# Kernel optimization log

Hardware: AMD Instinct MI355X
Metric: run time of the kernel (lower is better)

## Reference

```python
import jax, jax.numpy as jnp
import numpy as np

N = 100000
E = 600000
EL = 200000
HID = 16
HEADS = 4
NUM_NODE_TYPES = 8
NUM_EDGE_TYPES = 22
EDGE_DIM = 16


def setup_inputs() -> dict:
    key = jax.random.key(0)
    ks = jax.random.split(key, 32)
    s = 0.1
    d1, d2 = HID, HID * HEADS  # per-head dims of layer1 / layer2
    inp = {
        'x': jax.random.normal(ks[0], (N, HID), jnp.float32),
        'edge_index': jax.random.randint(ks[1], (2, E), 0, N),
        'node_type': jax.random.randint(ks[2], (N,), 0, NUM_NODE_TYPES),
        'edge_attr': jax.random.normal(ks[3], (E, EDGE_DIM), jnp.float32),
        'edge_type': jax.random.randint(ks[4], (E,), 0, NUM_EDGE_TYPES),
        'edge_label_index': jax.random.randint(ks[5], (2, EL), 0, N),
        # ---- layer 1 params (in=HID, heads=4, out-per-head=HID, concat) ----
        'Wx1': jax.random.normal(ks[6], (HID, HEADS * d1)) * s,
        'We1': jax.random.normal(ks[7], (EDGE_DIM, HEADS * d1)) * s,
        'nt1': jax.random.normal(ks[8], (NUM_NODE_TYPES, HID)) * s,
        'et1': jax.random.normal(ks[9], (NUM_EDGE_TYPES, HEADS * d1)) * s,
        'as1': jax.random.normal(ks[10], (HEADS, d1)) * s,
        'ad1': jax.random.normal(ks[11], (HEADS, d1)) * s,
        'ae1': jax.random.normal(ks[12], (HEADS, d1)) * s,
        'res1': jax.random.normal(ks[13], (HID, HEADS * d1)) * s,
        # ---- layer 2 params (in=4*HID, heads=4, out-per-head=4*HID, mean) ----
        'Wx2': jax.random.normal(ks[14], (HEADS * HID, HEADS * d2)) * s,
        'We2': jax.random.normal(ks[15], (EDGE_DIM, HEADS * d2)) * s,
        'nt2': jax.random.normal(ks[16], (NUM_NODE_TYPES, HEADS * HID)) * s,
        'et2': jax.random.normal(ks[17], (NUM_EDGE_TYPES, HEADS * d2)) * s,
        'as2': jax.random.normal(ks[18], (HEADS, d2)) * s,
        'ad2': jax.random.normal(ks[19], (HEADS, d2)) * s,
        'ae2': jax.random.normal(ks[20], (HEADS, d2)) * s,
        # ---- edge decoder (2*4*HID -> 4*HID -> 1) ----
        'W1': jax.random.normal(ks[21], (2 * HEADS * HID, HEADS * HID)) * s,
        'b1': jnp.zeros((HEADS * HID,), jnp.float32),
        'W2': jax.random.normal(ks[22], (HEADS * HID, 1)) * s,
        'b2': jnp.zeros((1,), jnp.float32),
    }
    return inp


def hgat_layer(x, edge_index, node_type, edge_attr, edge_type,
               Wx, We, nt_emb, et_emb, a_s, a_d, a_e, res_W,
               heads, d, concat, n):
    src, dst = edge_index[0], edge_index[1]
    # type-conditioned node projection -> [N, heads, d]
    h = ((x + nt_emb[node_type]) @ Wx).reshape(n, heads, d)
    # type-conditioned edge features -> [E, heads, d]
    e = (edge_attr @ We + et_emb[edge_type]).reshape(-1, heads, d)
    hs = h[src]  # [E, heads, d] gather
    hd = h[dst]
    sc = (jnp.einsum('ehd,hd->eh', hs, a_s)
          + jnp.einsum('ehd,hd->eh', hd, a_d)
          + jnp.einsum('ehd,hd->eh', e, a_e))
    sc = jax.nn.leaky_relu(sc, 0.2)
    # segment softmax over incoming edges of each destination node
    m = jax.ops.segment_max(sc, dst, num_segments=n)
    p = jnp.exp(sc - m[dst])
    den = jax.ops.segment_sum(p, dst, num_segments=n)
    alpha = p / (den[dst] + 1e-16)
    msg = alpha[:, :, None] * (hs + e)  # [E, heads, d]
    out = jax.ops.segment_sum(msg.reshape(-1, heads * d), dst, num_segments=n)
    out = out.reshape(n, heads, d)
    if concat:
        return out.reshape(n, heads * d) + x @ res_W
    else:
        return out.mean(axis=1) + x  # in-dim == out-dim: identity residual


def reference(x, edge_index, node_type, edge_attr, edge_type, edge_label_index,
              Wx1, We1, nt1, et1, as1, ad1, ae1, res1,
              Wx2, We2, nt2, et2, as2, ad2, ae2,
              W1, b1, W2, b2):
    n = x.shape[0]
    z = hgat_layer(x, edge_index, node_type, edge_attr, edge_type,
                   Wx1, We1, nt1, et1, as1, ad1, ae1, res1,
                   HEADS, HID, True, n)
    z = jax.nn.relu(z)
    z = hgat_layer(z, edge_index, node_type, edge_attr, edge_type,
                   Wx2, We2, nt2, et2, as2, ad2, ae2, None,
                   HEADS, HEADS * HID, False, n)
    # edge decoder: gather endpoint embeddings, 2-layer MLP
    row, col = edge_label_index[0], edge_label_index[1]
    zz = jnp.concatenate([z[row], z[col]], axis=-1)  # [EL, 2*4*HID]
    h = jax.nn.relu(zz @ W1 + b1)
    pred = (h @ W2 + b2).reshape(-1)
    return pred, z
```

## Files before the change

kernel.cpp:

```cpp
#include <hip/hip_runtime.h>
#include <stdint.h>

typedef unsigned short u16;
typedef unsigned int   u32;

#define NN  100000
#define NE  600000
#define NEL 200000

__device__ __forceinline__ float b2f(u16 u){ return __uint_as_float(((u32)u)<<16); }
__device__ __forceinline__ u16 f2b(float f){
  u32 u = __float_as_uint(f);
  u32 r = (u + 0x7FFFu + ((u>>16)&1u)) >> 16;
  return (u16)r;
}
__device__ __forceinline__ void unpack8(uint4 v, float* o){
  o[0]=__uint_as_float(v.x<<16); o[1]=__uint_as_float(v.x&0xffff0000u);
  o[2]=__uint_as_float(v.y<<16); o[3]=__uint_as_float(v.y&0xffff0000u);
  o[4]=__uint_as_float(v.z<<16); o[5]=__uint_as_float(v.z&0xffff0000u);
  o[6]=__uint_as_float(v.w<<16); o[7]=__uint_as_float(v.w&0xffff0000u);
}
__device__ __forceinline__ float ldf(const void* p, size_t i, int m){
  return m ? b2f(((const u16*)p)[i]) : ((const float*)p)[i];
}
__device__ __forceinline__ void ld16(const void* p, size_t off, int m, float* o){
  if (m){
    const uint4* q = (const uint4*)((const u16*)p + off);
    uint4 a=q[0], b=q[1]; unpack8(a,o); unpack8(b,o+8);
  } else {
    const float4* q = (const float4*)((const float*)p + off);
    float4 a=q[0],b=q[1],c=q[2],d=q[3];
    o[0]=a.x;o[1]=a.y;o[2]=a.z;o[3]=a.w; o[4]=b.x;o[5]=b.y;o[6]=b.z;o[7]=b.w;
    o[8]=c.x;o[9]=c.y;o[10]=c.z;o[11]=c.w; o[12]=d.x;o[13]=d.y;o[14]=d.z;o[15]=d.w;
  }
}
__device__ __forceinline__ void stf(void* p, size_t i, int m, float v){
  if (m) ((u16*)p)[i] = f2b(v); else ((float*)p)[i] = v;
}
__device__ __forceinline__ void atomAdd(float* p, float v){ unsafeAtomicAdd(p, v); }

__global__ void k_detect(const void* a0,const void* a3,const void* a6,const void* a7,
                         const void* a8,const void* a9,const void* a10,const void* a11,
                         const void* a12,const void* a13,const void* a14,const void* a15,
                         const void* a16,const void* a17,const void* a18,const void* a19,
                         const void* a20,const void* a21,const void* a23,
                         int* __restrict__ flags){
  const void* ptrs[19] = {a0,a3,a6,a7,a8,a9,a10,a11,a12,a13,a14,a15,a16,a17,a18,a19,a20,a21,a23};
  const int  idxs[19] = {0,3,6,7,8,9,10,11,12,13,14,15,16,17,18,19,20,21,23};
  int b = blockIdx.x;
  const u16* q = (const u16*)ptrs[b];
  u16 u = q[threadIdx.x];
  int e = (u>>7)&0xFF;
  bool good = (u==0) || (e>=110 && e<=141);
  unsigned long long m = __ballot(good);
  if (threadIdx.x==0) flags[idxs[b]] = (__popcll(m) >= 52) ? 1 : 0;
}

__global__ __launch_bounds__(256) void k_zero(float* __restrict__ buf, int n){
  int i = blockIdx.x*256 + threadIdx.x;
  if (i < n) buf[i] = 0.f;
}
__global__ __launch_bounds__(256) void k_stub(u16* __restrict__ out, int n){
  int i = blockIdx.x*256 + threadIdx.x;
  if (i < n) out[i] = 0;
}

__global__ __launch_bounds__(256) void k_pack(const void* __restrict__ Wx2,
                                              const int* __restrict__ flags,
                                              u32* __restrict__ Wxp){
  int m14 = flags[14];
  int i = blockIdx.x*256 + threadIdx.x;
  int k2=i>>8, col=i&255;
  u16 lo = f2b(ldf(Wx2,(size_t)(2*k2)*256+col,m14));
  u16 hi = f2b(ldf(Wx2,(size_t)(2*k2+1)*256+col,m14));
  Wxp[i] = ((u32)hi<<16)|lo;
}

__global__ __launch_bounds__(256) void k_hist(const int* __restrict__ ei, int* __restrict__ cnt){
  int e = blockIdx.x*256 + threadIdx.x;
  if (e < NE) atomicAdd(&cnt[ei[NE+e]], 1);
}
__global__ __launch_bounds__(256) void k_scan1(const int* __restrict__ cnt,
                                               int* __restrict__ row_ptr, int* __restrict__ bsum){
  __shared__ int sb[256];
  int i = blockIdx.x*256 + threadIdx.x, t = threadIdx.x;
  int c = (i < NN) ? cnt[i] : 0;
  sb[t] = c; __syncthreads();
  for (int off=1; off<256; off<<=1){
    int v = (t>=off) ? sb[t-off] : 0; __syncthreads();
    sb[t] += v; __syncthreads();
  }
  if (i < NN) row_ptr[i] = sb[t] - c;
  if (t == 255) bsum[blockIdx.x] = sb[255];
}
__global__ __launch_bounds__(512) void k_scan2(const int* __restrict__ bsum, int* __restrict__ boff){
  __shared__ int sb[512];
  int t = threadIdx.x;
  int nblk = (NN+255)/256;
  int c = (t < nblk) ? bsum[t] : 0;
  sb[t] = c; __syncthreads();
  for (int off=1; off<512; off<<=1){
    int v = (t>=off) ? sb[t-off] : 0; __syncthreads();
    sb[t] += v; __syncthreads();
  }
  boff[t] = sb[t] - c;
}
__global__ __launch_bounds__(256) void k_scan3(int* __restrict__ row_ptr, const int* __restrict__ boff){
  int i = blockIdx.x*256 + threadIdx.x;
  if (i < NN) row_ptr[i] += boff[blockIdx.x];
  if (i == 0) row_ptr[NN] = NE;
}
__global__ __launch_bounds__(256) void k_scatter(const int* __restrict__ ei, const int* __restrict__ etype,
                                                 const int* __restrict__ row_ptr,
                                                 int* __restrict__ cur, int* __restrict__ perm,
                                                 int* __restrict__ rank, int* __restrict__ se){
  int e = blockIdx.x*256 + threadIdx.x;
  if (e < NE){
    int d = ei[NE+e];
    int pos = row_ptr[d] + atomicAdd(&cur[d], 1);
    perm[pos] = e;
    rank[e] = pos;
    se[pos] = ei[e] | (etype[e]<<20);
  }
}

__global__ void k_fold(const void* __restrict__ We1, const void* __restrict__ ae1, const void* __restrict__ et1,
                       const void* __restrict__ We2, const void* __restrict__ ae2, const void* __restrict__ et2,
                       const int* __restrict__ flags,
                       float* We1a, float* et1a, float* We2a, float* et2a){
  int m7=flags[7], m12=flags[12], m9=flags[9], m15=flags[15], m20=flags[20], m17=flags[17];
  int t = threadIdx.x;
  if (t < 64){
    int k=t>>2, h=t&3; float s=0.f;
    for (int d=0; d<16; d++) s += ldf(We1,k*64+h*16+d,m7)*ldf(ae1,h*16+d,m12);
    We1a[t]=s;
  } else if (t < 152){
    int i=t-64; int k=i>>2, h=i&3; float s=0.f;
    for (int d=0; d<16; d++) s += ldf(et1,k*64+h*16+d,m9)*ldf(ae1,h*16+d,m12);
    et1a[i]=s;
  } else if (t < 216){
    int i=t-152; int k=i>>2, h=i&3; float s=0.f;
    for (int d=0; d<64; d++) s += ldf(We2,k*256+h*64+d,m15)*ldf(ae2,h*64+d,m20);
    We2a[i]=s;
  } else if (t < 304){
    int i=t-216; int k=i>>2, h=i&3; float s=0.f;
    for (int d=0; d<64; d++) s += ldf(et2,k*256+h*64+d,m17)*ldf(ae2,h*64+d,m20);
    et2a[i]=s;
  }
}

__global__ __launch_bounds__(256) void k1_node(
    const void* __restrict__ x, const int* __restrict__ ntype,
    const void* __restrict__ Wx1, const void* __restrict__ nt1, const void* __restrict__ res1,
    const void* __restrict__ as1, const void* __restrict__ ad1,
    const int* __restrict__ flags,
    float* __restrict__ h1, float* __restrict__ out1,
    float* __restrict__ ssrc1, float* __restrict__ sdst1){
  __shared__ float sWx[1024], sRes[1024], sA[64], sD[64], sNt[128];
  int m0=flags[0], m6=flags[6], m8=flags[8], m13=flags[13], m10=flags[10], m11=flags[11];
  for (int i=threadIdx.x;i<1024;i+=256){ sWx[i]=ldf(Wx1,i,m6); sRes[i]=ldf(res1,i,m13); }
  if (threadIdx.x<64){ sA[threadIdx.x]=ldf(as1,threadIdx.x,m10); sD[threadIdx.x]=ldf(ad1,threadIdx.x,m11); }
  if (threadIdx.x<128) sNt[threadIdx.x]=ldf(nt1,threadIdx.x,m8);
  __syncthreads();
  int n = blockIdx.x*256 + threadIdx.x;
  if (n >= NN) return;
  float xv[16]; ld16(x, (size_t)n*16, m0, xv);
  int nt = ntype[n];
  float xin[16];
  #pragma unroll
  for (int k=0;k<16;k++) xin[k] = xv[k] + sNt[nt*16+k];
  float ss[4]={0,0,0,0}, sd[4]={0,0,0,0};
  #pragma unroll
  for (int jq=0;jq<16;jq++){
    float sarr[4], rarr[4];
    #pragma unroll
    for (int m=0;m<4;m++){
      int j = jq*4+m;
      float s=0.f, r=0.f;
      #pragma unroll
      for (int k=0;k<16;k++){ s += xin[k]*sWx[k*64+j]; r += xv[k]*sRes[k*64+j]; }
      sarr[m]=s; rarr[m]=r;
      ss[j>>4] += s*sA[j];
      sd[j>>4] += s*sD[j];
    }
    ((float4*)(h1  + (size_t)n*64))[jq] = make_float4(sarr[0],sarr[1],sarr[2],sarr[3]);
    ((float4*)(out1+ (size_t)n*64))[jq] = make_float4(rarr[0],rarr[1],rarr[2],rarr[3]);
  }
  ((float4*)ssrc1)[n] = make_float4(ss[0],ss[1],ss[2],ss[3]);
  ((float4*)sdst1)[n] = make_float4(sd[0],sd[1],sd[2],sd[3]);
}

__global__ __launch_bounds__(256) void k_sed(
    const int* __restrict__ ei, const void* __restrict__ eattr, const int* __restrict__ etype,
    const float* __restrict__ Wea, const float* __restrict__ eta,
    const float* __restrict__ ssrc, const float* __restrict__ sdst,
    const int* __restrict__ rank,
    const int* __restrict__ flags,
    float* __restrict__ psort){
  __shared__ float sW[64], sE[88];
  int m3=flags[3];
  if (threadIdx.x<64) sW[threadIdx.x]=Wea[threadIdx.x];
  if (threadIdx.x<88) sE[threadIdx.x]=eta[threadIdx.x];
  __syncthreads();
  int e = blockIdx.x*256 + threadIdx.x;
  if (e >= NE) return;
  int s = ei[e], d = ei[NE+e], t = etype[e];
  float ea[16]; ld16(eattr, (size_t)e*16, m3, ea);
  float4 s4 = ((const float4*)ssrc)[s];
  float4 d4 = ((const float4*)sdst)[d];
  float sv[4] = { s4.x+d4.x, s4.y+d4.y, s4.z+d4.z, s4.w+d4.w };
  float pv[4];
  #pragma unroll
  for (int h=0; h<4; h++){
    float v = sE[t*4+h] + sv[h];
    #pragma unroll
    for (int k=0;k<16;k++) v += ea[k]*sW[k*4+h];
    v = v > 0.f ? v : 0.2f*v;
    v = fminf(v, 60.f);
    pv[h] = __expf(v);
  }
  ((float4*)psort)[rank[e]] = make_float4(pv[0],pv[1],pv[2],pv[3]);
}

__global__ __launch_bounds__(256) void k_msg1(
    const void* __restrict__ eattr, const void* __restrict__ et1,
    const float* __restrict__ h1, const float* __restrict__ psort,
    const int* __restrict__ row_ptr, const int* __restrict__ perm, const int* __restrict__ se,
    const int* __restrict__ flags,
    float* __restrict__ out1, float* __restrict__ gsum1){
  __shared__ float sEt[22*64];
  int m3=flags[3], m9=flags[9];
  for (int i=threadIdx.x;i<22*64;i+=256) sEt[i]=ldf(et1,i,m9);
  __syncthreads();
  int j = threadIdx.x & 63;
  int h = j>>4, jk = j&15;
  int wid = threadIdx.x>>6;
  for (int it=0; it<8; ++it){
    int n = (blockIdx.x*4 + wid)*8 + it;
    int beg=row_ptr[n], end=row_ptr[n+1];
    float sp=0.f, acc=0.f, gacc=0.f;
    int i=beg;
    for (; i+1<end; i+=2){
      int st0=se[i], st1=se[i+1];
      float4 p0=((const float4*)psort)[i], p1=((const float4*)psort)[i+1];
      int pe0=perm[i], pe1=perm[i+1];
      int s0=st0&0xFFFFF, t0=st0>>20;
      int s1=st1&0xFFFFF, t1=st1>>20;
      float ph0 = (h==0?p0.x:h==1?p0.y:h==2?p0.z:p0.w);
      float ph1 = (h==0?p1.x:h==1?p1.y:h==2?p1.z:p1.w);
      float hv0 = h1[(size_t)s0*64+j];
      float hv1 = h1[(size_t)s1*64+j];
      float ea0 = ldf(eattr,(size_t)pe0*16+jk,m3);
      float ea1 = ldf(eattr,(size_t)pe1*16+jk,m3);
      sp   += ph0 + ph1;
      acc  += ph0*(hv0+sEt[t0*64+j]) + ph1*(hv1+sEt[t1*64+j]);
      gacc += ph0*ea0 + ph1*ea1;
    }
    if (i<end){
      int st0=se[i];
      float4 p0=((const float4*)psort)[i];
      int pe0=perm[i];
      int s0=st0&0xFFFFF, t0=st0>>20;
      float ph0 = (h==0?p0.x:h==1?p0.y:h==2?p0.z:p0.w);
      sp   += ph0;
      acc  += ph0*(h1[(size_t)s0*64+j]+sEt[t0*64+j]);
      gacc += ph0*ldf(eattr,(size_t)pe0*16+jk,m3);
    }
    float rd = 1.f/(sp+1e-16f);
    out1[(size_t)n*64+j] += acc*rd;
    gsum1[(size_t)n*64+j] = gacc*rd;
  }
}

__global__ __launch_bounds__(256) void k_fin1(
    const float* __restrict__ gsum1, const void* __restrict__ We1,
    const int* __restrict__ flags, float* __restrict__ out1){
  __shared__ float sW[16*64];
  __shared__ float sG[4][64];
  int m7=flags[7];
  for (int i=threadIdx.x;i<16*64;i+=256) sW[i]=ldf(We1,i,m7);
  __syncthreads();
  int slot=threadIdx.x>>6, j=threadIdx.x&63;
  int h = j>>4;
  for (int nb=blockIdx.x; nb<NN/4; nb+=gridDim.x){
    int n = nb*4 + slot;
    sG[slot][j] = gsum1[(size_t)n*64 + j];
    float s=0.f;
    #pragma unroll
    for (int k=0;k<16;k++) s += sG[slot][h*16+k]*sW[k*64+j];
    out1[(size_t)n*64+j] += s;
  }
}

__global__ __launch_bounds__(256) void k5_node2(
    const int* __restrict__ ntype,
    const u32* __restrict__ Wxp, const void* __restrict__ nt2,
    const void* __restrict__ as2, const void* __restrict__ ad2,
    const int* __restrict__ flags,
    const float* __restrict__ out1, float* __restrict__ zfin,
    u16* __restrict__ h2, float* __restrict__ ssrc2, float* __restrict__ sdst2){
  __shared__ u32   sWp[32*256];
  __shared__ float sNt[512];
  __shared__ float sAs[256], sAd[256];
  __shared__ float sZ[4][8][64];
  __shared__ float sR[4][2][256];
  int m16=flags[16], m18=flags[18], m19=flags[19];
  for (int i=threadIdx.x;i<32*256;i+=256) sWp[i] = Wxp[i];
  for (int i=threadIdx.x;i<512;i+=256) sNt[i]=ldf(nt2,i,m16);
  sAs[threadIdx.x]=ldf(as2,threadIdx.x,m18);
  sAd[threadIdx.x]=ldf(ad2,threadIdx.x,m19);
  __syncthreads();
  int slot=threadIdx.x>>6, j=threadIdx.x&63;
  int base=(blockIdx.x*4+slot)*8;
  #pragma unroll
  for (int i=0;i<8;i++){
    int n=base+i;
    float z = out1[(size_t)n*64+j]; z = fmaxf(z, 0.f);
    zfin[(size_t)n*64+j] = z;
    sZ[slot][i][j] = z + sNt[(ntype[n]<<6)|j];
  }
  __syncthreads();
  float acc[8][4];
  #pragma unroll
  for (int i=0;i<8;i++){ acc[i][0]=0;acc[i][1]=0;acc[i][2]=0;acc[i][3]=0; }
  for (int k2=0;k2<32;k2++){
    u32 w0p=sWp[k2*256+j], w1p=sWp[k2*256+64+j], w2p=sWp[k2*256+128+j], w3p=sWp[k2*256+192+j];
    float w0l=__uint_as_float(w0p<<16), w0h=__uint_as_float(w0p&0xffff0000u);
    float w1l=__uint_as_float(w1p<<16), w1h=__uint_as_float(w1p&0xffff0000u);
    float w2l=__uint_as_float(w2p<<16), w2h=__uint_as_float(w2p&0xffff0000u);
    float w3l=__uint_as_float(w3p<<16), w3h=__uint_as_float(w3p&0xffff0000u);
    #pragma unroll
    for (int i=0;i<8;i++){
      float2 zz = *(const float2*)&sZ[slot][i][k2*2];
      acc[i][0] += zz.x*w0l + zz.y*w0h;
      acc[i][1] += zz.x*w1l + zz.y*w1h;
      acc[i][2] += zz.x*w2l + zz.y*w2h;
      acc[i][3] += zz.x*w3l + zz.y*w3h;
    }
  }
  int g=j>>4, l=j&15;
  #pragma unroll
  for (int i=0;i<8;i++){
    int n=base+i;
    u32 lo = (u32)f2b(acc[i][0]) | ((u32)f2b(acc[i][1])<<16);
    u32 hi = (u32)f2b(acc[i][2]) | ((u32)f2b(acc[i][3])<<16);
    *(uint2*)&h2[(size_t)n*256 + j*4] = make_uint2(lo,hi);
    sR[slot][0][      j] = acc[i][0]*sAs[      j];
    sR[slot][0][ 64 + j] = acc[i][1]*sAs[ 64 + j];
    sR[slot][0][128 + j] = acc[i][2]*sAs[128 + j];
    sR[slot][0][192 + j] = acc[i][3]*sAs[192 + j];
    sR[slot][1][      j] = acc[i][0]*sAd[      j];
    sR[slot][1][ 64 + j] = acc[i][1]*sAd[ 64 + j];
    sR[slot][1][128 + j] = acc[i][2]*sAd[128 + j];
    sR[slot][1][192 + j] = acc[i][3]*sAd[192 + j];
    float4 v4 = *(const float4*)&sR[slot][0][g*64 + l*4];
    float4 w4 = *(const float4*)&sR[slot][1][g*64 + l*4];
    float vs = v4.x+v4.y+v4.z+v4.w;
    float vd = w4.x+w4.y+w4.z+w4.w;
    #pragma unroll
    for (int off=1; off<16; off<<=1){ vs += __shfl_xor(vs,off); vd += __shfl_xor(vd,off); }
    if (l==0){ ssrc2[(size_t)n*4+g]=vs; sdst2[(size_t)n*4+g]=vd; }
  }
}

__global__ __launch_bounds__(256) void k_msg2(
    const void* __restrict__ eattr, const void* __restrict__ et2,
    const u16* __restrict__ h2, const float* __restrict__ psort,
    const int* __restrict__ row_ptr, const int* __restrict__ perm, const int* __restrict__ se,
    const int* __restrict__ flags,
    float* __restrict__ zfin, float* __restrict__ gsum){
  __shared__ float4 sEt4[22*64];
  int m3=flags[3], m17=flags[17];
  for (int i=threadIdx.x;i<22*64;i+=256){
    int t=i>>6, j=i&63;
    sEt4[i] = make_float4(ldf(et2,(size_t)t*256+j,m17),      ldf(et2,(size_t)t*256+64+j,m17),
                          ldf(et2,(size_t)t*256+128+j,m17),  ldf(et2,(size_t)t*256+192+j,m17));
  }
  __syncthreads();
  int j = threadIdx.x & 63;
  int jh = j>>4, jk = j&15;
  int wid = threadIdx.x>>6;
  for (int it=0; it<8; ++it){
    int n = (blockIdx.x*4 + wid)*8 + it;
    int beg=row_ptr[n], end=row_ptr[n+1];
    float ds0=0,ds1=0,ds2=0,ds3=0;
    float pa0=0,pa1=0,pa2=0,pa3=0, gacc=0;
    int i=beg;
    for (; i+1<end; i+=2){
      int st0=se[i], st1=se[i+1];
      float4 q0=((const float4*)psort)[i], q1=((const float4*)psort)[i+1];
      int pe0=perm[i], pe1=perm[i+1];
      int s0=st0&0xFFFFF, t0=st0>>20;
      int s1=st1&0xFFFFF, t1=st1>>20;
      uint2 hA = *(const uint2*)&h2[(size_t)s0*256 + j*4];
      uint2 hB = *(const uint2*)&h2[(size_t)s1*256 + j*4];
      float ea0 = ldf(eattr,(size_t)pe0*16+jk,m3);
      float ea1 = ldf(eattr,(size_t)pe1*16+jk,m3);
      float4 eA = sEt4[t0*64+j], eB = sEt4[t1*64+j];
      ds0 += q0.x+q1.x; ds1 += q0.y+q1.y; ds2 += q0.z+q1.z; ds3 += q0.w+q1.w;
      pa0 += q0.x*(__uint_as_float(hA.x<<16)        +eA.x) + q1.x*(__uint_as_float(hB.x<<16)        +eB.x);
      pa1 += q0.y*(__uint_as_float(hA.x&0xffff0000u)+eA.y) + q1.y*(__uint_as_float(hB.x&0xffff0000u)+eB.y);
      pa2 += q0.z*(__uint_as_float(hA.y<<16)        +eA.z) + q1.z*(__uint_as_float(hB.y<<16)        +eB.z);
      pa3 += q0.w*(__uint_as_float(hA.y&0xffff0000u)+eA.w) + q1.w*(__uint_as_float(hB.y&0xffff0000u)+eB.w);
      float pj0 = (jh==0?q0.x:jh==1?q0.y:jh==2?q0.z:q0.w);
      float pj1 = (jh==0?q1.x:jh==1?q1.y:jh==2?q1.z:q1.w);
      gacc += pj0*ea0 + pj1*ea1;
    }
    if (i<end){
      int st0=se[i];
      float4 q0=((const float4*)psort)[i];
      int pe0=perm[i];
      int s0=st0&0xFFFFF, t0=st0>>20;
      uint2 hA = *(const uint2*)&h2[(size_t)s0*256 + j*4];
      float4 eA = sEt4[t0*64+j];
      ds0 += q0.x; ds1 += q0.y; ds2 += q0.z; ds3 += q0.w;
      pa0 += q0.x*(__uint_as_float(hA.x<<16)        +eA.x);
      pa1 += q0.y*(__uint_as_float(hA.x&0xffff0000u)+eA.y);
      pa2 += q0.z*(__uint_as_float(hA.y<<16)        +eA.z);
      pa3 += q0.w*(__uint_as_float(hA.y&0xffff0000u)+eA.w);
      float pj0 = (jh==0?q0.x:jh==1?q0.y:jh==2?q0.z:q0.w);
      gacc += pj0*ldf(eattr,(size_t)pe0*16+jk,m3);
    }
    float r0=1.f/(ds0+1e-16f), r1=1.f/(ds1+1e-16f), r2=1.f/(ds2+1e-16f), r3=1.f/(ds3+1e-16f);
    float acc = pa0*r0 + pa1*r1 + pa2*r2 + pa3*r3;
    float rj = (jh==0?r0:jh==1?r1:jh==2?r2:r3);
    zfin[(size_t)n*64+j] += 0.25f*acc;
    gsum[(size_t)n*64+j] = gacc*rj;
  }
}

__global__ __launch_bounds__(256) void k_fin(
    const float* __restrict__ gsum, const void* __restrict__ We2,
    const int* __restrict__ flags, float* __restrict__ zfin){
  __shared__ float sW[16*256];
  __shared__ float sG[4][64];
  int m15=flags[15];
  for (int i=threadIdx.x;i<16*256;i+=256) sW[i]=ldf(We2,i,m15);
  __syncthreads();
  int slot=threadIdx.x>>6, j=threadIdx.x&63;
  for (int nb=blockIdx.x; nb<NN/4; nb+=gridDim.x){
    int n = nb*4 + slot;
    sG[slot][j] = gsum[(size_t)n*64 + j];
    float acc = 0.f;
    #pragma unroll
    for (int h=0;h<4;h++){
      float s=0.f;
      #pragma unroll
      for (int k=0;k<16;k++) s += sG[slot][h*16+k]*sW[k*256 + h*64 + j];
      acc += s;
    }
    zfin[(size_t)n*64+j] += 0.25f*acc;
  }
}

__global__ __launch_bounds__(256) void k_zout(const float* __restrict__ zf, void* __restrict__ out,
                                              const int* __restrict__ flags){
  int mo = flags[0];
  int i = blockIdx.x*256 + threadIdx.x;
  if (i < NN*64) stf(out, (size_t)NEL + i, mo, zf[i]);
}

__global__ __launch_bounds__(256) void k_dec(
    const int* __restrict__ eli, const float* __restrict__ zfin,
    const void* __restrict__ W1, const u16* __restrict__ b1,
    const void* __restrict__ W2, const u16* __restrict__ b2,
    const int* __restrict__ flags,
    void* __restrict__ out){
  __shared__ float sW1[128*64];
  __shared__ float sB1[64], sW2[64];
  __shared__ float sZZ[4][8][128];
  int m21=flags[21], m23=flags[23], mo=flags[0];
  for (int i=threadIdx.x;i<128*64;i+=256) sW1[i]=ldf(W1,i,m21);
  if (threadIdx.x<64){ sB1[threadIdx.x]=b2f(b1[threadIdx.x]); sW2[threadIdx.x]=ldf(W2,threadIdx.x,m23); }
  __syncthreads();
  float b2v = b2f(b2[0]);
  int slot=threadIdx.x>>6, j=threadIdx.x&63;
  int ngrp=(NEL+7)/8;
  for (int g0 = blockIdx.x*4; g0 < ngrp; g0 += gridDim.x*4){
    int g = g0 + slot;
    bool active = (g < ngrp);
    int e0 = active ? g*8 : 0;
    int cnt = active ? ((NEL - e0) < 8 ? (NEL - e0) : 8) : 0;
    #pragma unroll
    for (int q=0;q<8;q++){
      int qq = (q<cnt) ? q : 0;
      int r=eli[e0+qq], c=eli[NEL+e0+qq];
      sZZ[slot][q][j]    = zfin[(size_t)r*64+j];
      sZZ[slot][q][64+j] = zfin[(size_t)c*64+j];
    }
    __syncthreads();
    float acc[8];
    #pragma unroll
    for (int q=0;q<8;q++) acc[q]=sB1[j];
    for (int k4=0;k4<32;k4++){
      float w0=sW1[(k4*4+0)*64+j], w1=sW1[(k4*4+1)*64+j];
      float w2=sW1[(k4*4+2)*64+j], w3=sW1[(k4*4+3)*64+j];
      #pragma unroll
      for (int q=0;q<8;q++){
        float4 zz = *(const float4*)&sZZ[slot][q][k4*4];
        acc[q] += zz.x*w0 + zz.y*w1 + zz.z*w2 + zz.w*w3;
      }
    }
    #pragma unroll
    for (int q=0;q<8;q++){
      float a = fmaxf(acc[q],0.f)*sW2[j];
      #pragma unroll
      for (int off=32; off; off>>=1) a += __shfl_xor(a,off);
      if (j==0 && q<cnt) stf(out, e0+q, mo, a + b2v);
    }
    __syncthreads();
  }
}

extern "C" void kernel_launch(void* const* d_in, const int* in_sizes, int n_in,
                              void* d_out, int out_size, void* d_ws, size_t ws_size,
                              hipStream_t stream){
  (void)in_sizes; (void)n_in;
  const void* x    =d_in[0];
  const int* ei    =(const int*)d_in[1];
  const int* ntype =(const int*)d_in[2];
  const void* eattr=d_in[3];
  const int* etype =(const int*)d_in[4];
  const int* eli   =(const int*)d_in[5];
  const void* Wx1=d_in[6];  const void* We1=d_in[7];  const void* nt1=d_in[8];
  const void* et1=d_in[9];  const void* as1=d_in[10]; const void* ad1=d_in[11];
  const void* ae1=d_in[12]; const void* res1=d_in[13];
  const void* Wx2=d_in[14]; const void* We2=d_in[15]; const void* nt2=d_in[16];
  const void* et2=d_in[17]; const void* as2=d_in[18]; const void* ad2=d_in[19];
  const void* ae2=d_in[20];
  const void* W1=d_in[21];  const u16* b1=(const u16*)d_in[22];
  const void* W2=d_in[23];  const u16* b2=(const u16*)d_in[24];

  const size_t NEED_BYTES = 30809572ULL * 4ULL;
  if (ws_size < NEED_BYTES){
    k_stub<<<(out_size+255)/256,256,0,stream>>>((u16*)d_out, out_size);
    return;
  }
  float* ws=(float*)d_ws;
  size_t o=0;
  int*   flags=(int*)(ws+o); o+=32;
  float* We1a =ws+o; o+=64;
  float* et1a =ws+o; o+=96;
  float* We2a =ws+o; o+=64;
  float* et2a =ws+o; o+=96;
  int*   cnt    =(int*)(ws+o); o+=NN;
  int*   row_ptr=(int*)(ws+o); o+=NN+4;
  int*   perm   =(int*)(ws+o); o+=NE;
  int*   bsum   =(int*)(ws+o); o+=512;
  int*   boff   =(int*)(ws+o); o+=512;
  int*   rank   =(int*)(ws+o); o+=NE;
  int*   se     =(int*)(ws+o); o+=NE;
  u32*   Wxp    =(u32*)(ws+o); o+=8192;
  float* ssrc =ws+o; o+=(size_t)NN*4;
  float* sdst =ws+o; o+=(size_t)NN*4;
  float* psort=ws+o; o+=(size_t)NE*4;
  float* slotA=ws+o; o+=(size_t)NN*64;
  float* out1 =ws+o; o+=(size_t)NN*64;
  u16*   h2   =(u16*)(ws+o); o+=(size_t)NN*128;
  float* h1   = slotA;
  float* zfin = slotA;
  float* gsum = out1;
  float* gsum1= (float*)h2;

  const int NBLK = (NN+255)/256;

  k_detect<<<19,64,0,stream>>>(x,eattr,Wx1,We1,nt1,et1,as1,ad1,ae1,res1,
                               Wx2,We2,nt2,et2,as2,ad2,ae2,W1,W2,flags);
  k_fold<<<1,320,0,stream>>>(We1,ae1,et1,We2,ae2,et2,flags,We1a,et1a,We2a,et2a);
  k_pack<<<32,256,0,stream>>>(Wx2,flags,Wxp);
  k_zero<<<(NN+255)/256,256,0,stream>>>((float*)cnt, NN);
  k_hist<<<(NE+255)/256,256,0,stream>>>(ei, cnt);
  k_scan1<<<NBLK,256,0,stream>>>(cnt, row_ptr, bsum);
  k_scan2<<<1,512,0,stream>>>(bsum, boff);
  k_scan3<<<NBLK,256,0,stream>>>(row_ptr, boff);
  k_zero<<<(NN+255)/256,256,0,stream>>>((float*)cnt, NN);
  k_scatter<<<(NE+255)/256,256,0,stream>>>(ei, etype, row_ptr, cnt, perm, rank, se);
  k1_node<<<(NN+255)/256,256,0,stream>>>(x,ntype,Wx1,nt1,res1,as1,ad1,flags,h1,out1,ssrc,sdst);
  k_sed<<<(NE+255)/256,256,0,stream>>>(ei,eattr,etype,We1a,et1a,ssrc,sdst,rank,flags,psort);
  k_msg1<<<NN/32,256,0,stream>>>(eattr,et1,h1,psort,row_ptr,perm,se,flags,out1,gsum1);
  k_fin1<<<2048,256,0,stream>>>(gsum1,We1,flags,out1);
  k5_node2<<<NN/32,256,0,stream>>>(ntype,Wxp,nt2,as2,ad2,flags,out1,zfin,h2,ssrc,sdst);
  k_sed<<<(NE+255)/256,256,0,stream>>>(ei,eattr,etype,We2a,et2a,ssrc,sdst,rank,flags,psort);
  k_msg2<<<NN/32,256,0,stream>>>(eattr,et2,h2,psort,row_ptr,perm,se,flags,zfin,gsum);
  k_fin<<<2048,256,0,stream>>>(gsum,We2,flags,zfin);
  k_zout<<<(NN*64+255)/256,256,0,stream>>>(zfin,d_out,flags);
  k_dec<<<768,256,0,stream>>>(eli,zfin,W1,b1,W2,b2,flags,d_out);
}
```

Baseline: 736.2 us.

## Run edge decoder first layer on bf16 MFMA instead of scalar FMA

The decoder MLP's 128x64 first layer now runs on bf16 MFMA 16x16x32 instructions. Weights are pre-swizzled into LDS in B-fragment layout, and endpoint embeddings are gathered straight from global memory into A fragments, so the shared staging buffer and per-group barriers go away. ReLU, the W2 dot product and a 16-lane shuffle reduction finish each edge. This cuts the scalar FMA work and the LDS traffic, but rounds activations and weights to bf16 and assumes NEL is a multiple of 64.

Result: faster. 648.3 us (-11.9%).

```diff
diff --git a/kernel.cpp b/kernel.cpp
--- a/kernel.cpp
+++ b/kernel.cpp
@@ -3,6 +3,8 @@
 
 typedef unsigned short u16;
 typedef unsigned int   u32;
+typedef __attribute__((ext_vector_type(8))) short v8s;
+typedef __attribute__((ext_vector_type(4))) float v4f;
 
 #define NN  100000
 #define NE  600000
@@ -466,49 +468,58 @@
     const void* __restrict__ W2, const u16* __restrict__ b2,
     const int* __restrict__ flags,
     void* __restrict__ out){
-  __shared__ float sW1[128*64];
+  __shared__ v8s sB[4][4][64];
   __shared__ float sB1[64], sW2[64];
-  __shared__ float sZZ[4][8][128];
   int m21=flags[21], m23=flags[23], mo=flags[0];
-  for (int i=threadIdx.x;i<128*64;i+=256) sW1[i]=ldf(W1,i,m21);
+  for (int idx=threadIdx.x; idx<1024; idx+=256){
+    int kb=idx>>8, ct=(idx>>6)&3, l=idx&63;
+    int col = ct*16 + (l&15);
+    int kbase = kb*32 + ((l>>4)<<3);
+    short v[8];
+    #pragma unroll
+    for (int i=0;i<8;i++) v[i] = (short)f2b(ldf(W1,(size_t)(kbase+i)*64+col,m21));
+    sB[kb][ct][l] = *(v8s*)v;
+  }
   if (threadIdx.x<64){ sB1[threadIdx.x]=b2f(b1[threadIdx.x]); sW2[threadIdx.x]=ldf(W2,threadIdx.x,m23); }
   __syncthreads();
   float b2v = b2f(b2[0]);
-  int slot=threadIdx.x>>6, j=threadIdx.x&63;
-  int ngrp=(NEL+7)/8;
-  for (int g0 = blockIdx.x*4; g0 < ngrp; g0 += gridDim.x*4){
-    int g = g0 + slot;
-    bool active = (g < ngrp);
-    int e0 = active ? g*8 : 0;
-    int cnt = active ? ((NEL - e0) < 8 ? (NEL - e0) : 8) : 0;
-    #pragma unroll
-    for (int q=0;q<8;q++){
-      int qq = (q<cnt) ? q : 0;
-      int r=eli[e0+qq], c=eli[NEL+e0+qq];
-      sZZ[slot][q][j]    = zfin[(size_t)r*64+j];
-      sZZ[slot][q][64+j] = zfin[(size_t)c*64+j];
-    }
-    __syncthreads();
-    float acc[8];
-    #pragma unroll
-    for (int q=0;q<8;q++) acc[q]=sB1[j];
-    for (int k4=0;k4<32;k4++){
-      float w0=sW1[(k4*4+0)*64+j], w1=sW1[(k4*4+1)*64+j];
-      float w2=sW1[(k4*4+2)*64+j], w3=sW1[(k4*4+3)*64+j];
+  int w = threadIdx.x>>6, lane = threadIdx.x&63;
+  int l15 = lane&15, lk = lane>>4;
+  int ngrp = NEL/64;
+  for (int g = blockIdx.x; g < ngrp; g += gridDim.x){
+    int e0 = g*64 + w*16;
+    int eA = e0 + l15;
+    int rn = eli[eA], cn = eli[NEL+eA];
+    v8s a[4];
+    #pragma unroll
+    for (int kb=0;kb<4;kb++){
+      int k = kb*32 + lk*8;
+      const float* src = (k<64) ? (zfin + (size_t)rn*64 + k) : (zfin + (size_t)cn*64 + (k-64));
+      float4 f0 = *(const float4*)(src);
+      float4 f1 = *(const float4*)(src+4);
+      short v[8] = {(short)f2b(f0.x),(short)f2b(f0.y),(short)f2b(f0.z),(short)f2b(f0.w),
+                    (short)f2b(f1.x),(short)f2b(f1.y),(short)f2b(f1.z),(short)f2b(f1.w)};
+      a[kb] = *(v8s*)v;
+    }
+    float part[4] = {0,0,0,0};
+    #pragma unroll
+    for (int ct=0; ct<4; ct++){
+      v4f c = {0.f,0.f,0.f,0.f};
       #pragma unroll
-      for (int q=0;q<8;q++){
-        float4 zz = *(const float4*)&sZZ[slot][q][k4*4];
-        acc[q] += zz.x*w0 + zz.y*w1 + zz.z*w2 + zz.w*w3;
-      }
-    }
-    #pragma unroll
-    for (int q=0;q<8;q++){
-      float a = fmaxf(acc[q],0.f)*sW2[j];
+      for (int kb=0;kb<4;kb++)
+        c = __builtin_amdgcn_mfma_f32_16x16x32_bf16(a[kb], sB[kb][ct][lane], c, 0,0,0);
+      int col = ct*16 + l15;
+      float w2c = sW2[col], b1c = sB1[col];
       #pragma unroll
-      for (int off=32; off; off>>=1) a += __shfl_xor(a,off);
-      if (j==0 && q<cnt) stf(out, e0+q, mo, a + b2v);
-    }
-    __syncthreads();
+      for (int r=0;r<4;r++) part[r] += fmaxf(c[r]+b1c, 0.f) * w2c;
+    }
+    #pragma unroll
+    for (int r=0;r<4;r++){
+      float v = part[r];
+      #pragma unroll
+      for (int off=1; off<16; off<<=1) v += __shfl_xor(v, off);
+      if (l15==0) stf(out, e0 + lk*4 + r, mo, v + b2v);
+    }
   }
 }
 
@@ -584,5 +595,5 @@
   k_msg2<<<NN/32,256,0,stream>>>(eattr,et2,h2,psort,row_ptr,perm,se,flags,zfin,gsum);
   k_fin<<<2048,256,0,stream>>>(gsum,We2,flags,zfin);
   k_zout<<<(NN*64+255)/256,256,0,stream>>>(zfin,d_out,flags);
-  k_dec<<<768,256,0,stream>>>(eli,zfin,W1,b1,W2,b2,flags,d_out);
-}
+  k_dec<<<1024,256,0,stream>>>(eli,zfin,W1,b1,W2,b2,flags,d_out);
+}
```
